# Performance work log

Hardware: AMD Instinct MI355X
Metric: run time of the kernel (lower is better)

Reference implementation:

```python
import jax, jax.numpy as jnp
import numpy as np

B, C_IN, H, W = 64, 32, 28, 28
K = 5                       # receptive field
OH, OW = H - K + 1, W - K + 1  # 24, 24 (padding=0, stride=1)
C_OUT = 128
IN_SIZE = C_IN * K * K      # 800


def setup_inputs() -> dict:
    key = jax.random.key(0)
    ks = jax.random.split(key, 7)
    x = jax.random.uniform(ks[0], (B, C_IN, H, W), dtype=jnp.float32)
    # per-output-channel tree params: layer sizes 36 -> 6 -> 1, 6 inputs/node, 64-entry LUTs
    map1 = jax.random.randint(ks[1], (C_OUT, 36, 6), 0, IN_SIZE, dtype=jnp.int32)
    lut1 = jax.random.uniform(ks[2], (C_OUT, 36, 64), dtype=jnp.float32)
    map2 = jax.random.randint(ks[3], (C_OUT, 6, 6), 0, 36, dtype=jnp.int32)
    lut2 = jax.random.uniform(ks[4], (C_OUT, 6, 64), dtype=jnp.float32)
    map3 = jax.random.randint(ks[5], (C_OUT, 1, 6), 0, 6, dtype=jnp.int32)
    lut3 = jax.random.uniform(ks[6], (C_OUT, 1, 64), dtype=jnp.float32)
    return {"x": x, "map1": map1, "lut1": lut1, "map2": map2,
            "lut2": lut2, "map3": map3, "lut3": lut3}


def _lut_eval(xin, lut):
    # xin: [P, N, 6] soft bits in [0,1]; lut: [N, 64] LUT entries.
    # out[p,n] = sum_a lut[n,a] * prod_j (x_j if bit_j(a) else 1-x_j)
    P, N, k = xin.shape
    p = jnp.ones((P, N, 1), xin.dtype)
    for j in range(k):  # build address probabilities incrementally; peak [P,N,64]
        xj = xin[:, :, j]
        pair = jnp.stack([1.0 - xj, xj], axis=-1)          # [P,N,2]
        p = (p[:, :, :, None] * pair[:, :, None, :]).reshape(P, N, -1)
    return jnp.einsum('pna,na->pn', p, lut)


def _unfold(x):
    # im2col, kernel 5, stride 1, no padding -> [B*OH*OW, C_IN*K*K]
    patches = jax.lax.conv_general_dilated_patches(
        x, (K, K), (1, 1), 'VALID')                        # [B, C*K*K, OH, OW]
    patches = patches.transpose(0, 2, 3, 1).reshape(-1, IN_SIZE)
    return patches


def _forward(x, map1, lut1, map2, lut2, map3, lut3):
    patches = _unfold(x)                                   # [P, 800]

    def tree(_, params):  # one output channel's LUT tree (chunked in torch code)
        m1, l1, m2, l2, m3, l3 = params
        h = jnp.clip(_lut_eval(patches[:, m1], l1), 0.0, 1.0)  # [P,36]
        h = jnp.clip(_lut_eval(h[:, m2], l2), 0.0, 1.0)        # [P,6]
        h = jnp.clip(_lut_eval(h[:, m3], l3), 0.0, 1.0)        # [P,1]
        return None, h[:, 0]

    _, outs = jax.lax.scan(tree, None, (map1, lut1, map2, lut2, map3, lut3))
    # outs: [C_OUT, P] -> [B, C_OUT, OH, OW]
    out = outs.T.reshape(B, OH * OW, C_OUT).transpose(0, 2, 1)
    return out.reshape(B, C_OUT, OH, OW)


def reference(x, map1, lut1, map2, lut2, map3, lut3):
    return _forward(x, map1, lut1, map2, lut2, map3, lut3)
```

## Files before the change

kernel.cpp:

```cpp
#include <hip/hip_runtime.h>

#define B_      64
#define CIN     32
#define H_      28
#define W_      28
#define OH_     24
#define OW_     24
#define COUT    128
#define NPOS    (OH_ * OW_)
#define HW_     (H_ * W_)
#define XSTRIDE (CIN * HW_)
#define BHALF   32

#define BLOCK    256
#define NLANES   (BHALF * NPOS)
#define UBLOCKS  (NLANES / BLOCK)
#define TPB      2
#define NTP      64
#define TGROUPS  (NTP / TPB)
#define NXCD     8
#define UPX      (UBLOCKS / NXCD)

#define CF4_PER_TP (43 * 32)
#define OFF_INTS   (NTP * 36 * 12)
#define COEF_FLTS  (NTP * 43 * 128)
#define WS_NEEDED  ((OFF_INTS + COEF_FLTS) * 4)

typedef float f2 __attribute__((ext_vector_type(2)));
typedef float f4 __attribute__((ext_vector_type(4)));
struct p2 { f2 a, b; };

__device__ __forceinline__ f2 pkfma(f2 x, f2 h, f2 l) {
    return __builtin_elementwise_fma(x, h, l);
}

__device__ __forceinline__ f2 clamp2(f2 v) {
    f2 r;
    r.x = __builtin_amdgcn_fmed3f(v.x, 0.0f, 1.0f);
    r.y = __builtin_amdgcn_fmed3f(v.y, 0.0f, 1.0f);
    return r;
}

template<int M>
struct RecL {
    static __device__ __forceinline__ p2 go(const f4* __restrict__ C, int a0,
                                            const p2* xs) {
        p2 lo = RecL<M - 1>::go(C, a0, xs);
        p2 hi = RecL<M - 1>::go(C, a0 + (1 << (M - 2)), xs);
        p2 r;
        r.a = pkfma(xs[6 - M].a, hi.a, lo.a);
        r.b = pkfma(xs[6 - M].b, hi.b, lo.b);
        return r;
    }
};
template<>
struct RecL<1> {
    static __device__ __forceinline__ p2 go(const f4* __restrict__ C, int a0,
                                            const p2* xs) {
        f4 q = C[a0];
        f2 lo; lo.x = q.x; lo.y = q.y;
        f2 hi; hi.x = q.z; hi.y = q.w;
        p2 r;
        r.a = pkfma(xs[5].a, hi, lo);
        r.b = pkfma(xs[5].b, hi, lo);
        return r;
    }
};

__device__ __forceinline__ p2 contract2(const f4* __restrict__ C, const p2 xs[6]) {
    p2 r = RecL<6>::go(C, 0, xs);
    r.a = clamp2(r.a);
    r.b = clamp2(r.b);
    return r;
}

__global__ __launch_bounds__(BLOCK, 3)
void lutconv_l(const float* __restrict__ x,
               const int* __restrict__ OFFS,
               const f4* __restrict__ COEF,
               float* __restrict__ out) {
    __shared__ f4 CLs[CF4_PER_TP];

    const int bid = blockIdx.x;
    const int xcd = bid % NXCD;
    const int j   = bid / NXCD;
    const int tg  = j % TGROUPS;
    const int us  = j / TGROUPS;
    const int u   = xcd * UPX + us;

    const int g   = u * BLOCK + threadIdx.x;
    const int b0  = g / NPOS;
    const int pos = g - b0 * NPOS;
    const int oh  = pos / OW_;
    const int ow  = pos - oh * OW_;
    const unsigned lin   = oh * W_ + ow;
    const unsigned voff0 = (b0 * XSTRIDE + lin) * 4u;
    const unsigned voff1 = voff0 + BHALF * XSTRIDE * 4u;
    const char* xc = (const char*)x;

#pragma unroll 1
    for (int tpi = 0; tpi < TPB; ++tpi) {
        const int tp = tg * TPB + tpi;

        if (tpi) __syncthreads();
        {
            const f4* src = COEF + (size_t)tp * CF4_PER_TP;
#pragma unroll
            for (int k = 0; k < 6; ++k) {
                int i = k * BLOCK + threadIdx.x;
                if (i < CF4_PER_TP) CLs[i] = src[i];
            }
        }
        __syncthreads();

        const int* Ot = OFFS + tp * (36 * 12);

        p2 h2[6];
#pragma unroll
        for (int j3 = 0; j3 < 6; ++j3) {
            p2 h1[6];
#pragma unroll
            for (int j1 = 0; j1 < 6; ++j1) {
                const int* oi = Ot + (j3 * 6 + j1) * 12;
                p2 xs[6];
#pragma unroll
                for (int jj = 0; jj < 6; ++jj) {
                    int o0 = __builtin_amdgcn_readfirstlane(oi[2 * jj]);
                    int o1 = __builtin_amdgcn_readfirstlane(oi[2 * jj + 1]);
                    f2 va, vb;
                    va.x = *(const float*)(xc + o0 + voff0);
                    va.y = *(const float*)(xc + o1 + voff0);
                    vb.x = *(const float*)(xc + o0 + voff1);
                    vb.y = *(const float*)(xc + o1 + voff1);
                    xs[jj].a = va;
                    xs[jj].b = vb;
                }
                h1[j1] = contract2(&CLs[(j3 * 7 + j1) * 32], xs);
            }
            h2[j3] = contract2(&CLs[(j3 * 7 + 6) * 32], h1);
        }
        p2 r = contract2(&CLs[42 * 32], h2);

        size_t ob = ((size_t)b0 * COUT + 2 * tp) * NPOS + pos;
        out[ob]        = r.a.x;
        out[ob + NPOS] = r.a.y;
        size_t ob2 = ob + (size_t)BHALF * COUT * NPOS;
        out[ob2]        = r.b.x;
        out[ob2 + NPOS] = r.b.y;
    }
}

__global__ void prep(const int* __restrict__ map1, const float* __restrict__ lut1,
                     const int* __restrict__ map2, const float* __restrict__ lut2,
                     const int* __restrict__ map3, const float* __restrict__ lut3,
                     int* __restrict__ OFFS, float* __restrict__ COEF) {
    const int rec  = blockIdx.x % 43;
    const int tp   = blockIdx.x / 43;
    const int lane = threadIdx.x;
    const int t0 = 2 * tp, t1 = 2 * tp + 1;

    const float* lp0;
    const float* lp1;
    int node;
    if (rec == 42) {
        node = 42;
        lp0 = lut3 + t0 * 64;
        lp1 = lut3 + t1 * 64;
    } else {
        const int j3 = rec / 7;
        const int jr = rec - 7 * j3;
        const int n20 = map3[t0 * 6 + j3];
        const int n21 = map3[t1 * 6 + j3];
        if (jr == 6) {
            node = j3 * 7 + 6;
            lp0 = lut2 + (t0 * 6 + n20) * 64;
            lp1 = lut2 + (t1 * 6 + n21) * 64;
        } else {
            const int n10 = map2[(t0 * 6 + n20) * 6 + jr];
            const int n11 = map2[(t1 * 6 + n21) * 6 + jr];
            node = j3 * 7 + jr;
            lp0 = lut1 + (t0 * 36 + n10) * 64;
            lp1 = lut1 + (t1 * 36 + n11) * 64;
            if (lane < 12) {
                int h  = lane & 1;
                int jj = lane >> 1;
                int n1 = h ? n11 : n10;
                int t  = h ? t1 : t0;
                int m  = map1[(t * 36 + n1) * 6 + jj];
                int c  = m / 25;
                int r  = m - 25 * c;
                int kh = r / 5;
                int kw = r - 5 * kh;
                OFFS[(tp * 36 + j3 * 6 + jr) * 12 + jj * 2 + h] =
                    (c * HW_ + kh * W_ + kw) * 4;
            }
        }
    }

    float c0 = lp0[lane];
    float c1 = lp1[lane];
#pragma unroll
    for (int s = 1; s < 64; s <<= 1) {
        float o0 = __shfl_xor(c0, s);
        float o1 = __shfl_xor(c1, s);
        if (lane & s) { c0 -= o0; c1 -= o1; }
    }
    float* cp = COEF + ((size_t)tp * 43 + node) * 128;
    int slot = (lane >> 1) * 4 + (lane & 1) * 2;
    cp[slot]     = c0;
    cp[slot + 1] = c1;
}

__device__ __forceinline__ float clamp01(float v) {
    return __builtin_amdgcn_fmed3f(v, 0.0f, 1.0f);
}

__device__ __forceinline__ float contract64s(const float* __restrict__ L,
                                             const float xs[6]) {
    float v[32];
#pragma unroll
    for (int a = 0; a < 32; ++a) {
        float b = L[2 * a];
        v[a] = fmaf(xs[5], L[2 * a + 1] - b, b);
    }
#pragma unroll
    for (int a = 0; a < 16; ++a) v[a] = fmaf(xs[4], v[2*a+1] - v[2*a], v[2*a]);
#pragma unroll
    for (int a = 0; a < 8; ++a)  v[a] = fmaf(xs[3], v[2*a+1] - v[2*a], v[2*a]);
#pragma unroll
    for (int a = 0; a < 4; ++a)  v[a] = fmaf(xs[2], v[2*a+1] - v[2*a], v[2*a]);
#pragma unroll
    for (int a = 0; a < 2; ++a)  v[a] = fmaf(xs[1], v[2*a+1] - v[2*a], v[2*a]);
    return clamp01(fmaf(xs[0], v[1] - v[0], v[0]));
}

__global__ __launch_bounds__(BLOCK, 4)
void lutconv_fb(const float* __restrict__ x,
                const int* __restrict__ map1, const float* __restrict__ lut1,
                const int* __restrict__ map2, const float* __restrict__ lut2,
                const int* __restrict__ map3, const float* __restrict__ lut3,
                float* __restrict__ out) {
    const int g   = (blockIdx.x % 144) * BLOCK + threadIdx.x;
    const int tg  = blockIdx.x / 144;
    const int b   = g / NPOS;
    const int pos = g - b * NPOS;
    const int lin = (pos / OW_) * W_ + (pos - (pos / OW_) * OW_);
    const float* xb = x + (size_t)b * XSTRIDE;

#pragma unroll 1
    for (int tt = 0; tt < 8; ++tt) {
        const int t = tg * 8 + tt;
        float h2[6];
#pragma unroll
        for (int j3 = 0; j3 < 6; ++j3) {
            int n2 = __builtin_amdgcn_readfirstlane(map3[t * 6 + j3]);
            float h1[6];
#pragma unroll
            for (int j1 = 0; j1 < 6; ++j1) {
                int n1 = __builtin_amdgcn_readfirstlane(map2[(t * 6 + n2) * 6 + j1]);
                float xs[6];
#pragma unroll
                for (int jj = 0; jj < 6; ++jj) {
                    int m = map1[(t * 36 + n1) * 6 + jj];
                    int c = m / 25, r = m - 25 * c, kh = r / 5, kw = r - 5 * kh;
                    int off = __builtin_amdgcn_readfirstlane(c * HW_ + kh * W_ + kw);
                    xs[jj] = xb[off + lin];
                }
                h1[j1] = contract64s(lut1 + (t * 36 + n1) * 64, xs);
            }
            h2[j3] = contract64s(lut2 + (t * 6 + n2) * 64, h1);
        }
        out[((size_t)b * COUT + t) * NPOS + pos] = contract64s(lut3 + t * 64, h2);
    }
}

extern "C" void kernel_launch(void* const* d_in, const int* in_sizes, int n_in,
                              void* d_out, int out_size, void* d_ws, size_t ws_size,
                              hipStream_t stream) {
    const float* x    = (const float*)d_in[0];
    const int*   map1 = (const int*)d_in[1];
    const float* lut1 = (const float*)d_in[2];
    const int*   map2 = (const int*)d_in[3];
    const float* lut2 = (const float*)d_in[4];
    const int*   map3 = (const int*)d_in[5];
    const float* lut3 = (const float*)d_in[6];
    float* out = (float*)d_out;

    if (ws_size >= (size_t)WS_NEEDED) {
        int*   OFFS = (int*)d_ws;
        float* COEF = (float*)((char*)d_ws + OFF_INTS * 4);
        prep<<<NTP * 43, 64, 0, stream>>>(map1, lut1, map2, lut2, map3, lut3,
                                          OFFS, COEF);
        lutconv_l<<<UBLOCKS * TGROUPS, BLOCK, 0, stream>>>(
            x, OFFS, (const f4*)COEF, out);
    } else {
        lutconv_fb<<<144 * 16, BLOCK, 0, stream>>>(
            x, map1, lut1, map2, lut2, map3, lut3, out);
    }
}
```

Baseline: 433.4 us.

## Interleave batch pairs of input and pack four positions per thread over one channel

Adds a prep pass that interleaves batch b and b+32 of x into float2 pairs, so each gather fetches two batch values with one 8-byte load. The main kernel now gives each thread four batch samples for a single output channel instead of two samples for two channels. It stages the Mobius coefficients of two channels in shared memory once per block, with 192-thread blocks. The old paired-channel path is kept as a fallback, but the new path needs a larger workspace and an extra pass over x.

Result: slower. 460.5 us (+6.3%).

```diff
diff --git a/kernel.cpp b/kernel.cpp
--- a/kernel.cpp
+++ b/kernel.cpp
@@ -10,21 +10,33 @@
 #define NPOS    (OH_ * OW_)
 #define HW_     (H_ * W_)
 #define XSTRIDE (CIN * HW_)
-#define BHALF   32
+#define PSTRIDE (CIN * HW_)
+
+#define BLK      192
+#define NQ       16
+#define NLANES   (NQ * NPOS)
+#define UB       (NLANES / BLK)
+#define TPB      2
+#define TG       (COUT / TPB)
+#define NXCD     8
+#define UPX      (UB / NXCD)
+
+#define XP_BYTES   (32 * PSTRIDE * 8)
+#define OFF_BYTES  (COUT * 36 * 6 * 4)
+#define COEF_BYTES (COUT * 43 * 64 * 4)
+#define WS_NEW     (XP_BYTES + OFF_BYTES + COEF_BYTES)
 
 #define BLOCK    256
-#define NLANES   (BHALF * NPOS)
-#define UBLOCKS  (NLANES / BLOCK)
-#define TPB      2
+#define BHALF    32
+#define NLANES6  (BHALF * NPOS)
+#define UBLOCKS6 (NLANES6 / BLOCK)
+#define TPB6     2
 #define NTP      64
-#define TGROUPS  (NTP / TPB)
-#define NXCD     8
-#define UPX      (UBLOCKS / NXCD)
-
+#define TGROUPS6 (NTP / TPB6)
+#define UPX6     (UBLOCKS6 / NXCD)
 #define CF4_PER_TP (43 * 32)
-#define OFF_INTS   (NTP * 36 * 12)
-#define COEF_FLTS  (NTP * 43 * 128)
-#define WS_NEEDED  ((OFF_INTS + COEF_FLTS) * 4)
+#define OFF6_INTS  (NTP * 36 * 12)
+#define WS_R6      ((OFF6_INTS + NTP * 43 * 128) * 4)
 
 typedef float f2 __attribute__((ext_vector_type(2)));
 typedef float f4 __attribute__((ext_vector_type(4)));
@@ -39,6 +51,175 @@
     r.x = __builtin_amdgcn_fmed3f(v.x, 0.0f, 1.0f);
     r.y = __builtin_amdgcn_fmed3f(v.y, 0.0f, 1.0f);
     return r;
+}
+
+template<int I>
+__device__ __forceinline__ f2 sp(f4 q) {
+    return __builtin_shufflevector(q, q, I, I);
+}
+
+template<int M>
+struct RecT {
+    static __device__ __forceinline__ p2 go(const float* __restrict__ C, int a0,
+                                            const p2* xs) {
+        p2 lo = RecT<M - 1>::go(C, a0, xs);
+        p2 hi = RecT<M - 1>::go(C, a0 + (1 << (M - 2)), xs);
+        p2 r;
+        r.a = pkfma(xs[6 - M].a, hi.a, lo.a);
+        r.b = pkfma(xs[6 - M].b, hi.b, lo.b);
+        return r;
+    }
+};
+template<>
+struct RecT<2> {
+    static __device__ __forceinline__ p2 go(const float* __restrict__ C, int a0,
+                                            const p2* xs) {
+        f4 q = *(const f4*)(C + 2 * a0);
+        p2 v0, v1, r;
+        v0.a = pkfma(xs[5].a, sp<1>(q), sp<0>(q));
+        v0.b = pkfma(xs[5].b, sp<1>(q), sp<0>(q));
+        v1.a = pkfma(xs[5].a, sp<3>(q), sp<2>(q));
+        v1.b = pkfma(xs[5].b, sp<3>(q), sp<2>(q));
+        r.a = pkfma(xs[4].a, v1.a, v0.a);
+        r.b = pkfma(xs[4].b, v1.b, v0.b);
+        return r;
+    }
+};
+
+__device__ __forceinline__ p2 contractT(const float* __restrict__ C, const p2 xs[6]) {
+    p2 r = RecT<6>::go(C, 0, xs);
+    r.a = clamp2(r.a);
+    r.b = clamp2(r.b);
+    return r;
+}
+
+__global__ __launch_bounds__(BLK, 3)
+void lutconv_x(const char* __restrict__ xpc,
+               const int* __restrict__ OFFS,
+               const float* __restrict__ COEF,
+               float* __restrict__ out) {
+    __shared__ float CLs[TPB * 43 * 64];
+
+    const int bid = blockIdx.x;
+    const int xcd = bid % NXCD;
+    const int j   = bid / NXCD;
+    const int tg  = j % TG;
+    const int usl = j / TG;
+    const int us  = xcd * UPX + usl;
+
+    const int g   = us * BLK + threadIdx.x;
+    const int bq  = g / NPOS;
+    const int pos = g - bq * NPOS;
+    const int oh  = pos / OW_;
+    const int ow  = pos - oh * OW_;
+    const unsigned lin   = oh * W_ + ow;
+    const unsigned byteA = (bq * PSTRIDE + lin) * 8u;
+    const unsigned byteB = ((bq + 16) * PSTRIDE + lin) * 8u;
+
+    {
+        const f4* src = (const f4*)(COEF + (size_t)tg * (TPB * 43 * 64));
+        f4* dst = (f4*)CLs;
+#pragma unroll
+        for (int k = 0; k < 8; ++k) {
+            int i = k * BLK + threadIdx.x;
+            if (i < TPB * 43 * 16) dst[i] = src[i];
+        }
+    }
+    __syncthreads();
+
+#pragma unroll 1
+    for (int tt = 0; tt < TPB; ++tt) {
+        const int t = tg * TPB + tt;
+        const float* Ct = CLs + tt * (43 * 64);
+        const int* Ot = OFFS + t * (36 * 6);
+
+        p2 h2[6];
+#pragma unroll
+        for (int j3 = 0; j3 < 6; ++j3) {
+            p2 h1[6];
+#pragma unroll
+            for (int j1 = 0; j1 < 6; ++j1) {
+                const int* oi = Ot + (j3 * 6 + j1) * 6;
+                p2 xs[6];
+#pragma unroll
+                for (int jj = 0; jj < 6; ++jj) {
+                    int o = __builtin_amdgcn_readfirstlane(oi[jj]);
+                    const char* p = xpc + o;
+                    p2 w;
+                    w.a = *(const f2*)(p + byteA);
+                    w.b = *(const f2*)(p + byteB);
+                    xs[jj] = w;
+                }
+                h1[j1] = contractT(Ct + (j3 * 7 + j1) * 64, xs);
+            }
+            h2[j3] = contractT(Ct + (j3 * 7 + 6) * 64, h1);
+        }
+        p2 r = contractT(Ct + 42 * 64, h2);
+
+        const size_t istr = (size_t)16 * COUT * NPOS;
+        size_t o0 = ((size_t)bq * COUT + t) * NPOS + pos;
+        out[o0]            = r.a.x;
+        out[o0 + 2 * istr] = r.a.y;
+        out[o0 + istr]     = r.b.x;
+        out[o0 + 3 * istr] = r.b.y;
+    }
+}
+
+__global__ void prep_xp(const float* __restrict__ x, f2* __restrict__ xp) {
+    int i = blockIdx.x * 256 + threadIdx.x;
+    if (i < 32 * PSTRIDE) {
+        int p = i / PSTRIDE;
+        int r = i - p * PSTRIDE;
+        f2 v;
+        v.x = x[p * XSTRIDE + r];
+        v.y = x[(p + 32) * XSTRIDE + r];
+        xp[i] = v;
+    }
+}
+
+__global__ void prep_cf(const int* __restrict__ map1, const float* __restrict__ lut1,
+                        const int* __restrict__ map2, const float* __restrict__ lut2,
+                        const int* __restrict__ map3, const float* __restrict__ lut3,
+                        int* __restrict__ OFFS, float* __restrict__ COEF) {
+    const int rec  = blockIdx.x % 43;
+    const int t    = blockIdx.x / 43;
+    const int lane = threadIdx.x;
+
+    const float* lp;
+    int node;
+    if (rec == 42) {
+        node = 42;
+        lp = lut3 + t * 64;
+    } else {
+        const int j3 = rec / 7;
+        const int jr = rec - 7 * j3;
+        const int n2 = map3[t * 6 + j3];
+        if (jr == 6) {
+            node = j3 * 7 + 6;
+            lp = lut2 + (t * 6 + n2) * 64;
+        } else {
+            const int n1 = map2[(t * 6 + n2) * 6 + jr];
+            node = j3 * 7 + jr;
+            lp = lut1 + (t * 36 + n1) * 64;
+            if (lane < 6) {
+                int m  = map1[(t * 36 + n1) * 6 + lane];
+                int c  = m / 25;
+                int r  = m - 25 * c;
+                int kh = r / 5;
+                int kw = r - 5 * kh;
+                OFFS[t * 216 + (j3 * 6 + jr) * 6 + lane] =
+                    (c * HW_ + kh * W_ + kw) * 8;
+            }
+        }
+    }
+
+    float cv = lp[lane];
+#pragma unroll
+    for (int s = 1; s < 64; s <<= 1) {
+        float o = __shfl_xor(cv, s);
+        if (lane & s) cv -= o;
+    }
+    COEF[((size_t)t * 43 + node) * 64 + lane] = cv;
 }
 
 template<int M>
@@ -84,9 +265,9 @@
     const int bid = blockIdx.x;
     const int xcd = bid % NXCD;
     const int j   = bid / NXCD;
-    const int tg  = j % TGROUPS;
-    const int us  = j / TGROUPS;
-    const int u   = xcd * UPX + us;
+    const int tg  = j % TGROUPS6;
+    const int us  = j / TGROUPS6;
+    const int u   = xcd * UPX6 + us;
 
     const int g   = u * BLOCK + threadIdx.x;
     const int b0  = g / NPOS;
@@ -99,8 +280,8 @@
     const char* xc = (const char*)x;
 
 #pragma unroll 1
-    for (int tpi = 0; tpi < TPB; ++tpi) {
-        const int tp = tg * TPB + tpi;
+    for (int tpi = 0; tpi < TPB6; ++tpi) {
+        const int tp = tg * TPB6 + tpi;
 
         if (tpi) __syncthreads();
         {
@@ -150,10 +331,10 @@
     }
 }
 
-__global__ void prep(const int* __restrict__ map1, const float* __restrict__ lut1,
-                     const int* __restrict__ map2, const float* __restrict__ lut2,
-                     const int* __restrict__ map3, const float* __restrict__ lut3,
-                     int* __restrict__ OFFS, float* __restrict__ COEF) {
+__global__ void prep_l(const int* __restrict__ map1, const float* __restrict__ lut1,
+                       const int* __restrict__ map2, const float* __restrict__ lut2,
+                       const int* __restrict__ map3, const float* __restrict__ lut3,
+                       int* __restrict__ OFFS, float* __restrict__ COEF) {
     const int rec  = blockIdx.x % 43;
     const int tp   = blockIdx.x / 43;
     const int lane = threadIdx.x;
@@ -286,12 +467,21 @@
     const float* lut3 = (const float*)d_in[6];
     float* out = (float*)d_out;
 
-    if (ws_size >= (size_t)WS_NEEDED) {
+    if (ws_size >= (size_t)WS_NEW) {
+        f2*    xp   = (f2*)d_ws;
+        int*   OFFS = (int*)((char*)d_ws + XP_BYTES);
+        float* COEF = (float*)((char*)d_ws + XP_BYTES + OFF_BYTES);
+
+        prep_xp<<<(32 * PSTRIDE + 255) / 256, 256, 0, stream>>>(x, xp);
+        prep_cf<<<COUT * 43, 64, 0, stream>>>(map1, lut1, map2, lut2, map3, lut3,
+                                              OFFS, COEF);
+        lutconv_x<<<UB * TG, BLK, 0, stream>>>((const char*)xp, OFFS, COEF, out);
+    } else if (ws_size >= (size_t)WS_R6) {
         int*   OFFS = (int*)d_ws;
-        float* COEF = (float*)((char*)d_ws + OFF_INTS * 4);
-        prep<<<NTP * 43, 64, 0, stream>>>(map1, lut1, map2, lut2, map3, lut3,
-                                          OFFS, COEF);
-        lutconv_l<<<UBLOCKS * TGROUPS, BLOCK, 0, stream>>>(
+        float* COEF = (float*)((char*)d_ws + OFF6_INTS * 4);
+        prep_l<<<NTP * 43, 64, 0, stream>>>(map1, lut1, map2, lut2, map3, lut3,
+                                            OFFS, COEF);
+        lutconv_l<<<UBLOCKS6 * TGROUPS6, BLOCK, 0, stream>>>(
             x, OFFS, (const f4*)COEF, out);
     } else {
         lutconv_fb<<<144 * 16, BLOCK, 0, stream>>>(
```
